# Performance work log

Measured on AMD Instinct MI355X. Metric: run time of the kernel, lower is better.

Reference implementation:

```python
import jax, jax.numpy as jnp
import numpy as np

B, Q, D = 8, 900, 256
NH, DH = 8, 32
FF = 1024
NLEVELS, NPOINTS, NLAYERS = 4, 4, 6
SHAPES = [(100, 100), (50, 50), (25, 25), (13, 13)]
S = sum(h * w for h, w in SHAPES)  # 13294
EPS = 1e-5
SCALE = 1.0 / float(np.sqrt(DH))


def layer_norm(x, g, b):
    mu = jnp.mean(x, -1, keepdims=True)
    var = jnp.var(x, -1, keepdims=True)
    return (x - mu) * jax.lax.rsqrt(var + EPS) * g + b


def mha(x, wi, bi, wo, bo):
    qkv = x @ wi.T + bi
    q, k, v = jnp.split(qkv, 3, axis=-1)
    q = q.reshape(B, Q, NH, DH)
    k = k.reshape(B, Q, NH, DH)
    v = v.reshape(B, Q, NH, DH)
    attn = jax.nn.softmax(jnp.einsum('bqhd,bkhd->bhqk', q, k) * SCALE, -1)
    o = jnp.einsum('bhqk,bkhd->bqhd', attn, v).reshape(B, Q, D)
    return o @ wo.T + bo


def msda_core(value, loc, aw):
    # value (B,S,NH,DH); loc (B,Q,NH,L,P,2) in [0,1]; aw (B,Q,NH,L,P)
    v = value.transpose(0, 2, 1, 3)  # (B,NH,S,DH)
    out = jnp.zeros((B, NH, Q, DH), value.dtype)
    start = 0
    for lvl, (H_, W_) in enumerate(SHAPES):
        vl = v[:, :, start:start + H_ * W_]  # (B,NH,HW,DH)
        start += H_ * W_
        l = loc[:, :, :, lvl].transpose(0, 2, 1, 3, 4).reshape(B, NH, Q * NPOINTS, 2)
        # grid_sample align_corners=False pixel coords
        x = l[..., 0] * W_ - 0.5
        y = l[..., 1] * H_ - 0.5
        x0 = jnp.floor(x)
        y0 = jnp.floor(y)
        wx = x - x0
        wy = y - y0
        g = jnp.zeros((B, NH, Q * NPOINTS, DH), value.dtype)
        for dy, dx, w in ((0, 0, (1 - wx) * (1 - wy)), (0, 1, wx * (1 - wy)),
                          (1, 0, (1 - wx) * wy), (1, 1, wx * wy)):
            xi = x0 + dx
            yi = y0 + dy
            valid = ((xi >= 0) & (xi < W_) & (yi >= 0) & (yi < H_)).astype(value.dtype)
            idx = (jnp.clip(yi, 0, H_ - 1) * W_ + jnp.clip(xi, 0, W_ - 1)).astype(jnp.int32)
            gi = jnp.take_along_axis(vl, idx[..., None], axis=2)  # (B,NH,QP,DH)
            g = g + gi * (w * valid)[..., None]
        g = g.reshape(B, NH, Q, NPOINTS, DH)
        a = aw[:, :, :, lvl].transpose(0, 2, 1, 3)  # (B,NH,Q,P)
        out = out + jnp.einsum('bhqpd,bhqp->bhqd', g, a)
    return out.transpose(0, 2, 1, 3).reshape(B, Q, D)


def msda(query, ref, value_in, vp_w, vp_b, so_w, so_b, aw_w, aw_b, op_w, op_b):
    value = (value_in @ vp_w.T + vp_b).reshape(B, S, NH, DH)
    off = (query @ so_w.T + so_b).reshape(B, Q, NH, NLEVELS, NPOINTS, 2)
    aw = (query @ aw_w.T + aw_b).reshape(B, Q, NH, NLEVELS * NPOINTS)
    aw = jax.nn.softmax(aw, -1).reshape(B, Q, NH, NLEVELS, NPOINTS)
    # offset normalizer is (W, H) per level
    norm = jnp.array([[w, h] for h, w in SHAPES], jnp.float32)
    loc = ref[:, :, None, :, None, :] + off / norm[None, None, None, :, None, :]
    return msda_core(value, loc, aw) @ op_w.T + op_b


def setup_inputs():
    key = jax.random.key(0)
    it = iter(jax.random.split(key, 32))

    def rn(shape, s=0.02):
        return jax.random.normal(next(it), shape, jnp.float32) * s

    z = lambda n: jnp.zeros((n,), jnp.float32)
    o = lambda n: jnp.ones((n,), jnp.float32)
    NOFF = NH * NLEVELS * NPOINTS
    return {
        'tgt': rn((B, Q, D), 1.0),
        'reference_points': jax.random.uniform(next(it), (B, Q, 2), jnp.float32),
        'memory': rn((B, S, D), 1.0),
        'spatial_shapes': jnp.array(SHAPES, jnp.int32),
        'level_start_index': jnp.array(np.cumsum([0] + [h * w for h, w in SHAPES[:-1]]), jnp.int32),
        'valid_ratios': jnp.ones((B, NLEVELS, 2), jnp.float32),
        'query_pos': rn((B, Q, D), 1.0),
        'sa_in_w': rn((3 * D, D)), 'sa_in_b': z(3 * D),
        'sa_out_w': rn((D, D)), 'sa_out_b': z(D),
        'n1_g': o(D), 'n1_b': z(D),
        'n2_g': o(D), 'n2_b': z(D),
        'n3_g': o(D), 'n3_b': z(D),
        'vp_w': rn((D, D)), 'vp_b': z(D),
        'so_w': rn((NOFF * 2, D)), 'so_b': rn((NOFF * 2,), 0.5),
        'aw_w': rn((NOFF, D)), 'aw_b': z(NOFF),
        'op_w': rn((D, D)), 'op_b': z(D),
        'ff1_w': rn((FF, D)), 'ff1_b': z(FF),
        'ff2_w': rn((D, FF)), 'ff2_b': z(D),
    }


def reference(tgt, reference_points, memory, spatial_shapes, level_start_index,
              valid_ratios, query_pos,
              sa_in_w, sa_in_b, sa_out_w, sa_out_b,
              n1_g, n1_b, n2_g, n2_b, n3_g, n3_b,
              vp_w, vp_b, so_w, so_b, aw_w, aw_b, op_w, op_b,
              ff1_w, ff1_b, ff2_w, ff2_b):
    # NOTE: nn.ModuleList([decoder_layer]*num_layers) in the source shares one
    # layer's weights across all 6 layers; bbox_embed is None so reference
    # points are constant across layers.
    output = tgt
    ref_input = reference_points[:, :, None, :] * valid_ratios[:, None, :, :]  # (B,Q,L,2)
    inter, inter_refs = [], []
    for _ in range(NLAYERS):
        output = output + query_pos
        t2 = mha(output, sa_in_w, sa_in_b, sa_out_w, sa_out_b)
        output = layer_norm(output + t2, n1_g, n1_b)
        t2 = msda(output, ref_input, memory, vp_w, vp_b, so_w, so_b, aw_w, aw_b, op_w, op_b)
        output = layer_norm(output + t2, n2_g, n2_b)
        t2 = jax.nn.relu(output @ ff1_w.T + ff1_b) @ ff2_w.T + ff2_b
        output = layer_norm(output + t2, n3_g, n3_b)
        inter.append(output)
        inter_refs.append(reference_points)
    return (jnp.stack(inter), jnp.stack(inter_refs))
```

## Files before the change

kernel.cpp:

```cpp
#include <hip/hip_runtime.h>
#include <hip/hip_bf16.h>

typedef __hip_bfloat16 bf16;
typedef __bf16 bf16x8 __attribute__((ext_vector_type(8)));
typedef float  f32x4  __attribute__((ext_vector_type(4)));

#define NB 8
#define NQ 900
#define DM 256
#define NHEADS 8
#define DHEAD 32
#define NFF 1024
#define NLAY 6
#define NS 13294
#define BQ (NB*NQ)
#define LN_EPS 1e-5f
#define ATT_SCALE 0.17677669529663687f
#define SAK 40
#define VWS 264
#define PSK 88

__device__ __forceinline__ float bfd(const bf16* p, size_t i){ return __bfloat162float(p[i]); }

__device__ __forceinline__ float ldv(const void* p, size_t i, int mode, bool extF32)
{
    if (mode == 0) return ((const float*)p)[i];
    if (mode == 1) return bfd((const bf16*)p, i);
    return extF32 ? ((const float*)p)[i] : bfd((const bf16*)p, i);
}

__device__ __forceinline__ void unpack8(uint4 u, float* t)
{
    t[0] = __uint_as_float((u.x & 0xffffu) << 16);
    t[1] = __uint_as_float(u.x & 0xffff0000u);
    t[2] = __uint_as_float((u.y & 0xffffu) << 16);
    t[3] = __uint_as_float(u.y & 0xffff0000u);
    t[4] = __uint_as_float((u.z & 0xffffu) << 16);
    t[5] = __uint_as_float(u.z & 0xffff0000u);
    t[6] = __uint_as_float((u.w & 0xffffu) << 16);
    t[7] = __uint_as_float(u.w & 0xffff0000u);
}

__global__ __launch_bounds__(256) void detect_dtype(const void* __restrict__ tgt,
        float* __restrict__ flag)
{
    __shared__ float red[256];
    int t = threadIdx.x;
    const unsigned short* u = (const unsigned short*)tgt;
    float m = 0.f;
    for (int i = t; i < 2048; i += 256) {
        unsigned int bits = ((unsigned int)u[i]) << 16;
        float v = fabsf(__uint_as_float(bits));
        if (!isfinite(v)) v = 1e30f;
        m = fmaxf(m, v);
    }
    red[t] = m;
    __syncthreads();
    for (int st = 128; st; st >>= 1) {
        if (t < st) red[t] = fmaxf(red[t], red[t + st]);
        __syncthreads();
    }
    if (t == 0) flag[0] = (red[0] > 1e8f) ? 1.f : 0.f;
}

__global__ __launch_bounds__(256) void convert_w(const void* __restrict__ src,
        bf16* __restrict__ dst, const float* __restrict__ flagp)
{
    const bool ef = flagp[0] > 0.5f;
    size_t base = ((size_t)blockIdx.x * 256 + threadIdx.x) * 8;
    if (ef) {
        const float* s = (const float*)src + base;
        float4 f0 = *(const float4*)s;
        float4 f1 = *(const float4*)(s + 4);
        union { bf16 a[8]; uint4 u; } t;
        t.a[0] = __float2bfloat16(f0.x); t.a[1] = __float2bfloat16(f0.y);
        t.a[2] = __float2bfloat16(f0.z); t.a[3] = __float2bfloat16(f0.w);
        t.a[4] = __float2bfloat16(f1.x); t.a[5] = __float2bfloat16(f1.y);
        t.a[6] = __float2bfloat16(f1.z); t.a[7] = __float2bfloat16(f1.w);
        *(uint4*)(dst + base) = t.u;
    } else {
        *(uint4*)(dst + base) = *(const uint4*)((const bf16*)src + base);
    }
}

__global__ __launch_bounds__(256, 2) void gemm_vp(const void* __restrict__ A,
        const bf16* __restrict__ Wb, const void* __restrict__ bias,
        bf16* __restrict__ C, int M, const float* __restrict__ flagp)
{
    const bool ef = flagp[0] > 0.5f;
    __shared__ __align__(16) bf16 Al[64 * VWS];
    const int tid = threadIdx.x;
    const int w = tid >> 6, lane = tid & 63, lm = lane & 15, lq = lane >> 4;
    const int wq = w * 64;

    bf16x8 wf[4][8];
    #pragma unroll
    for (int nt = 0; nt < 4; nt++)
        #pragma unroll
        for (int ks = 0; ks < 8; ks++)
            wf[nt][ks] = *(const bf16x8*)(Wb +
                (size_t)(wq + nt * 16 + lm) * 256 + ks * 32 + lq * 8);

    float bv[4];
    #pragma unroll
    for (int nt = 0; nt < 4; nt++) bv[nt] = ldv(bias, wq + nt * 16 + lm, 2, ef);

    const int arow_l = tid >> 2;
    const int asub   = tid & 3;

    const int ntiles = (M + 63) / 64;
    for (int tile = blockIdx.x; tile < ntiles; tile += gridDim.x) {
        const int m0 = tile * 64;
        __syncthreads();
        {
            const int grow = m0 + arow_l;
            if (grow < M) {
                if (ef) {
                    const float* ap = (const float*)A + (size_t)grow * 256;
                    #pragma unroll
                    for (int j = 0; j < 16; j++) {
                        int colf = j * 16 + asub * 4;
                        float4 f = *(const float4*)(ap + colf);
                        union { bf16 a[4]; uint2 u; } t;
                        t.a[0] = __float2bfloat16(f.x); t.a[1] = __float2bfloat16(f.y);
                        t.a[2] = __float2bfloat16(f.z); t.a[3] = __float2bfloat16(f.w);
                        *(uint2*)&Al[arow_l * VWS + colf] = t.u;
                    }
                } else {
                    const bf16* ap = (const bf16*)A + (size_t)grow * 256;
                    #pragma unroll
                    for (int j = 0; j < 8; j++) {
                        int cole = j * 32 + asub * 8;
                        *(uint4*)&Al[arow_l * VWS + cole] = *(const uint4*)(ap + cole);
                    }
                }
            } else {
                uint4 z = make_uint4(0u, 0u, 0u, 0u);
                #pragma unroll
                for (int j = 0; j < 8; j++)
                    *(uint4*)&Al[arow_l * VWS + j * 32 + asub * 8] = z;
            }
        }
        __syncthreads();

        f32x4 acc[4][4];
        #pragma unroll
        for (int mi = 0; mi < 4; mi++)
            #pragma unroll
            for (int nt = 0; nt < 4; nt++)
                acc[mi][nt] = (f32x4){0.f, 0.f, 0.f, 0.f};

        #pragma unroll
        for (int ks = 0; ks < 8; ks++) {
            bf16x8 af[4];
            #pragma unroll
            for (int mi = 0; mi < 4; mi++)
                af[mi] = *(const bf16x8*)&Al[(mi * 16 + lm) * VWS + ks * 32 + lq * 8];
            #pragma unroll
            for (int nt = 0; nt < 4; nt++)
                #pragma unroll
                for (int mi = 0; mi < 4; mi++)
                    acc[mi][nt] = __builtin_amdgcn_mfma_f32_16x16x32_bf16(
                                      af[mi], wf[nt][ks], acc[mi][nt], 0, 0, 0);
        }

        #pragma unroll
        for (int mi = 0; mi < 4; mi++) {
            #pragma unroll
            for (int r = 0; r < 4; r++) {
                int m = m0 + mi * 16 + lq * 4 + r;
                if (m >= M) continue;
                #pragma unroll
                for (int nt = 0; nt < 4; nt++) {
                    int col = wq + nt * 16 + lm;
                    C[(size_t)m * 256 + col] = __float2bfloat16(acc[mi][nt][r] + bv[nt]);
                }
            }
        }
    }
}

__device__ __forceinline__ void stage_a32(bf16* As, const void* A, bool a_bf16,
        int m0, int M, int K, int k0, int tid)
{
    const int row = tid >> 3, col = (tid & 7) * 4;
    const int arow = m0 + row;
    union { bf16 a[4]; uint2 u; } t;
    if (arow < M) {
        size_t base = (size_t)arow * K + k0 + col;
        if (a_bf16) {
            t.u = *(const uint2*)((const bf16*)A + base);
        } else {
            float4 f = *(const float4*)((const float*)A + base);
            t.a[0] = __float2bfloat16(f.x); t.a[1] = __float2bfloat16(f.y);
            t.a[2] = __float2bfloat16(f.z); t.a[3] = __float2bfloat16(f.w);
        }
    } else {
        t.u = make_uint2(0u, 0u);
    }
    *(uint2*)&As[row * SAK + col] = t.u;
}

__global__ __launch_bounds__(256) void gemm_a(const void* __restrict__ A, int amode,
        const bf16* __restrict__ Wb, const void* __restrict__ bias,
        void* __restrict__ C, int cmode, int M, int N, int K, int relu,
        const float* __restrict__ flagp)
{
    const bool ef = flagp[0] > 0.5f;
    const bool a_bf16 = (amode == 1) || (amode == 2 && !ef);
    __shared__ __align__(16) bf16 As[32 * SAK];
    __shared__ __align__(16) bf16 Ws[256 * SAK];
    const int tid = threadIdx.x;
    const int m0 = blockIdx.y * 32, n0 = blockIdx.x * 256;
    const int w = tid >> 6, lane = tid & 63, lm = lane & 15, lq = lane >> 4;
    const int wr = w >> 1, wc = w & 1;
    const int srow = tid >> 2, scol = (tid & 3) * 8;

    f32x4 acc[8];
    #pragma unroll
    for (int nt = 0; nt < 8; nt++) acc[nt] = (f32x4){0.f, 0.f, 0.f, 0.f};

    for (int k0 = 0; k0 < K; k0 += 32) {
        stage_a32(As, A, a_bf16, m0, M, K, k0, tid);
        #pragma unroll
        for (int it = 0; it < 4; it++) {
            int rr = it * 64 + srow;
            *(uint4*)&Ws[rr * SAK + scol] =
                *(const uint4*)(Wb + (size_t)(n0 + rr) * K + k0 + scol);
        }
        __syncthreads();

        bf16x8 af = *(const bf16x8*)&As[(wr * 16 + lm) * SAK + lq * 8];
        #pragma unroll
        for (int nt = 0; nt < 8; nt++) {
            bf16x8 bfr = *(const bf16x8*)&Ws[(wc * 128 + nt * 16 + lm) * SAK + lq * 8];
            acc[nt] = __builtin_amdgcn_mfma_f32_16x16x32_bf16(af, bfr, acc[nt], 0, 0, 0);
        }
        __syncthreads();
    }

    #pragma unroll
    for (int nt = 0; nt < 8; nt++) {
        int n = n0 + wc * 128 + nt * 16 + lm;
        float bv = ldv(bias, n, 2, ef);
        #pragma unroll
        for (int r = 0; r < 4; r++) {
            int m = m0 + wr * 16 + lq * 4 + r;
            if (m >= M) continue;
            float v = acc[nt][r] + bv;
            if (relu) v = fmaxf(v, 0.f);
            size_t ci = (size_t)m * N + n;
            if (cmode == 0) ((float*)C)[ci] = v;
            else            ((bf16*)C)[ci] = __float2bfloat16(v);
        }
    }
}

__global__ __launch_bounds__(256) void gemm_ln(const bf16* __restrict__ A,
        const bf16* __restrict__ Wb, const void* __restrict__ bias,
        const float* __restrict__ res, const void* __restrict__ gw,
        const void* __restrict__ bw, float* __restrict__ out32,
        bf16* __restrict__ outbf, void* __restrict__ dout, size_t obase,
        const void* __restrict__ qp, int M, int K,
        const float* __restrict__ flagp)
{
    const bool ef = flagp[0] > 0.5f;
    __shared__ __align__(16) bf16 As[32 * SAK];
    __shared__ __align__(16) bf16 Ws[256 * SAK];
    const int tid = threadIdx.x;
    const int m0 = blockIdx.y * 32;
    const int w = tid >> 6, lane = tid & 63, lm = lane & 15, lq = lane >> 4;
    const int wr = w >> 1, wc = w & 1;
    const int srow = tid >> 2, scol = (tid & 3) * 8;

    f32x4 acc[8];
    #pragma unroll
    for (int nt = 0; nt < 8; nt++) acc[nt] = (f32x4){0.f, 0.f, 0.f, 0.f};

    for (int k0 = 0; k0 < K; k0 += 32) {
        stage_a32(As, A, true, m0, M, K, k0, tid);
        #pragma unroll
        for (int it = 0; it < 4; it++) {
            int rr = it * 64 + srow;
            *(uint4*)&Ws[rr * SAK + scol] =
                *(const uint4*)(Wb + (size_t)rr * K + k0 + scol);
        }
        __syncthreads();

        bf16x8 af = *(const bf16x8*)&As[(wr * 16 + lm) * SAK + lq * 8];
        #pragma unroll
        for (int nt = 0; nt < 8; nt++) {
            bf16x8 bfr = *(const bf16x8*)&Ws[(wc * 128 + nt * 16 + lm) * SAK + lq * 8];
            acc[nt] = __builtin_amdgcn_mfma_f32_16x16x32_bf16(af, bfr, acc[nt], 0, 0, 0);
        }
        __syncthreads();
    }

    float bias_c[8], gcol[8], bcol[8];
    #pragma unroll
    for (int nt = 0; nt < 8; nt++) {
        int col = wc * 128 + nt * 16 + lm;
        bias_c[nt] = ldv(bias, col, 2, ef);
        gcol[nt]   = ldv(gw,   col, 2, ef);
        bcol[nt]   = ldv(bw,   col, 2, ef);
    }
    #pragma unroll
    for (int r = 0; r < 4; r++) {
        int row = m0 + wr * 16 + lq * 4 + r;
        bool vr_ = row < M;
        #pragma unroll
        for (int nt = 0; nt < 8; nt++) {
            int col = wc * 128 + nt * 16 + lm;
            float rv = vr_ ? res[(size_t)row * DM + col] : 0.f;
            acc[nt][r] += bias_c[nt] + rv;
        }
    }

    float* red = (float*)As;
    float mu[4], rstd[4];
    #pragma unroll
    for (int r = 0; r < 4; r++) {
        float s = 0.f;
        #pragma unroll
        for (int nt = 0; nt < 8; nt++) s += acc[nt][r];
        s += __shfl_xor(s, 1, 64); s += __shfl_xor(s, 2, 64);
        s += __shfl_xor(s, 4, 64); s += __shfl_xor(s, 8, 64);
        if (lm == 0) red[(wr * 16 + lq * 4 + r) * 2 + wc] = s;
    }
    __syncthreads();
    #pragma unroll
    for (int r = 0; r < 4; r++) {
        int rl = wr * 16 + lq * 4 + r;
        mu[r] = (red[rl * 2] + red[rl * 2 + 1]) * (1.f / DM);
    }
    #pragma unroll
    for (int r = 0; r < 4; r++) {
        float q = 0.f;
        #pragma unroll
        for (int nt = 0; nt < 8; nt++) {
            float d = acc[nt][r] - mu[r];
            q += d * d;
        }
        q += __shfl_xor(q, 1, 64); q += __shfl_xor(q, 2, 64);
        q += __shfl_xor(q, 4, 64); q += __shfl_xor(q, 8, 64);
        if (lm == 0) red[64 + (wr * 16 + lq * 4 + r) * 2 + wc] = q;
    }
    __syncthreads();
    #pragma unroll
    for (int r = 0; r < 4; r++) {
        int rl = wr * 16 + lq * 4 + r;
        float var = (red[64 + rl * 2] + red[64 + rl * 2 + 1]) * (1.f / DM);
        rstd[r] = rsqrtf(var + LN_EPS);
    }

    #pragma unroll
    for (int r = 0; r < 4; r++) {
        int row = m0 + wr * 16 + lq * 4 + r;
        if (row >= M) continue;
        size_t rbase = (size_t)row * DM;
        #pragma unroll
        for (int nt = 0; nt < 8; nt++) {
            int col = wc * 128 + nt * 16 + lm;
            float o = (acc[nt][r] - mu[r]) * rstd[r] * gcol[nt] + bcol[nt];
            if (dout) {
                if (ef) ((float*)dout)[obase + rbase + col] = o;
                else    ((bf16*)dout)[obase + rbase + col] = __float2bfloat16(o);
            }
            float o2 = o + (qp ? ldv(qp, rbase + col, 2, ef) : 0.f);
            out32[rbase + col] = o2;
            outbf[rbase + col] = __float2bfloat16(o2);
        }
    }
}

__global__ __launch_bounds__(256) void gemm_soaw(const bf16* __restrict__ A,
        const bf16* __restrict__ Wb, const void* __restrict__ b1,
        const void* __restrict__ b2, float* __restrict__ C1,
        float* __restrict__ C2, int M, const float* __restrict__ flagp)
{
    const bool ef = flagp[0] > 0.5f;
    const int K = DM;
    __shared__ __align__(16) bf16 As[32 * SAK];
    __shared__ __align__(16) bf16 Ws[128 * SAK];
    const int tid = threadIdx.x;
    const int m0 = blockIdx.y * 32, n0 = blockIdx.x * 128;
    const int w = tid >> 6, lane = tid & 63, lm = lane & 15, lq = lane >> 4;
    const int wr = w >> 1, wc = w & 1;
    const int srow = tid >> 2, scol = (tid & 3) * 8;

    f32x4 acc[4];
    #pragma unroll
    for (int nt = 0; nt < 4; nt++) acc[nt] = (f32x4){0.f, 0.f, 0.f, 0.f};

    for (int k0 = 0; k0 < K; k0 += 32) {
        stage_a32(As, A, true, m0, M, K, k0, tid);
        #pragma unroll
        for (int it = 0; it < 2; it++) {
            int rr = it * 64 + srow;
            *(uint4*)&Ws[rr * SAK + scol] =
                *(const uint4*)(Wb + (size_t)(n0 + rr) * K + k0 + scol);
        }
        __syncthreads();

        bf16x8 af = *(const bf16x8*)&As[(wr * 16 + lm) * SAK + lq * 8];
        #pragma unroll
        for (int nt = 0; nt < 4; nt++) {
            bf16x8 bfr = *(const bf16x8*)&Ws[(wc * 64 + nt * 16 + lm) * SAK + lq * 8];
            acc[nt] = __builtin_amdgcn_mfma_f32_16x16x32_bf16(af, bfr, acc[nt], 0, 0, 0);
        }
        __syncthreads();
    }

    float* Cd; const void* bsrc; int nst, c0;
    if (n0 < 256) { Cd = C1; bsrc = b1; nst = 256; c0 = n0; }
    else          { Cd = C2; bsrc = b2; nst = 128; c0 = n0 - 256; }

    #pragma unroll
    for (int nt = 0; nt < 4; nt++) {
        int cl = wc * 64 + nt * 16 + lm;
        float bv = ldv(bsrc, c0 + cl, 2, ef);
        #pragma unroll
        for (int r = 0; r < 4; r++) {
            int m = m0 + wr * 16 + lq * 4 + r;
            if (m >= M) continue;
            Cd[(size_t)m * nst + c0 + cl] = acc[nt][r] + bv;
        }
    }
}

__global__ __launch_bounds__(256) void add_qpos(const void* __restrict__ a, int amode,
        const void* __restrict__ qp, float* __restrict__ o, bf16* __restrict__ ob,
        const float* __restrict__ flagp)
{
    const bool ef = flagp[0] > 0.5f;
    int i = blockIdx.x * 256 + threadIdx.x;
    float v = ldv(a, i, amode, ef) + ldv(qp, i, 2, ef);
    o[i]  = v;
    ob[i] = __float2bfloat16(v);
}

__global__ __launch_bounds__(256) void mha_mfma(const bf16* __restrict__ qkv,
        bf16* __restrict__ out)
{
    const int qt = blockIdx.x, h = blockIdx.y, b = blockIdx.z;
    const int q0 = qt * 64;
    const int tid = threadIdx.x;
    const int w = tid >> 6, lane = tid & 63;
    const int lm = lane & 15, lq = lane >> 4;
    const int srow = tid >> 2, sc = (tid & 3) * 8;

    __shared__ __align__(16) bf16 Qs[64][SAK];
    __shared__ __align__(16) bf16 Ks[64][SAK];
    __shared__ __align__(16) bf16 Vt[32][66];
    __shared__ __align__(16) bf16 Ps[64][PSK];

    const bf16* base = qkv + (size_t)b * NQ * 768;

    {
        bf16 tmp[8];
        if (q0 + srow < NQ) {
            uint4 u = *(const uint4*)(base + (size_t)(q0 + srow) * 768 + h * DHEAD + sc);
            float t[8]; unpack8(u, t);
            #pragma unroll
            for (int i = 0; i < 8; i++) tmp[i] = __float2bfloat16(t[i] * ATT_SCALE);
        } else {
            #pragma unroll
            for (int i = 0; i < 8; i++) tmp[i] = __float2bfloat16(0.f);
        }
        *(uint4*)&Qs[srow][sc] = *(const uint4*)tmp;
    }
    __syncthreads();
    const bf16x8 qf = *(const bf16x8*)&Qs[w * 16 + lm][lq * 8];

    f32x4 O[2] = {{0.f,0.f,0.f,0.f},{0.f,0.f,0.f,0.f}};
    float mrow = -1e30f, lrow = 0.f;

    for (int k0 = 0; k0 < NQ; k0 += 64) {
        __syncthreads();
        {
            uint4 uk = {0u,0u,0u,0u}, uv = {0u,0u,0u,0u};
            if (k0 + srow < NQ) {
                const bf16* rp = base + (size_t)(k0 + srow) * 768 + h * DHEAD + sc;
                uk = *(const uint4*)(rp + 256);
                uv = *(const uint4*)(rp + 512);
            }
            *(uint4*)&Ks[srow][sc] = uk;
            const bf16* vv = (const bf16*)&uv;
            #pragma unroll
            for (int i = 0; i < 8; i++) Vt[sc + i][srow] = vv[i];
        }
        __syncthreads();

        float sv[16];
        #pragma unroll
        for (int mt = 0; mt < 4; mt++) {
            bf16x8 kf = *(const bf16x8*)&Ks[mt * 16 + lm][lq * 8];
            f32x4 d = __builtin_amdgcn_mfma_f32_16x16x32_bf16(kf, qf,
                        (f32x4){0.f,0.f,0.f,0.f}, 0, 0, 0);
            sv[mt*4+0] = d[0]; sv[mt*4+1] = d[1]; sv[mt*4+2] = d[2]; sv[mt*4+3] = d[3];
        }
        #pragma unroll
        for (int mt = 0; mt < 4; mt++)
            #pragma unroll
            for (int r = 0; r < 4; r++)
                if (k0 + mt * 16 + lq * 4 + r >= NQ) sv[mt*4+r] = -1e30f;

        float tmax = sv[0];
        #pragma unroll
        for (int j = 1; j < 16; j++) tmax = fmaxf(tmax, sv[j]);
        tmax = fmaxf(tmax, __shfl_xor(tmax, 16, 64));
        tmax = fmaxf(tmax, __shfl_xor(tmax, 32, 64));
        float mnew = fmaxf(mrow, tmax);
        float alpha = __expf(mrow - mnew);
        mrow = mnew;
        float psum = 0.f;
        #pragma unroll
        for (int j = 0; j < 16; j++) {
            float p = __expf(sv[j] - mnew);
            sv[j] = p; psum += p;
        }
        psum += __shfl_xor(psum, 16, 64);
        psum += __shfl_xor(psum, 32, 64);
        lrow = lrow * alpha + psum;

        #pragma unroll
        for (int mt = 0; mt < 4; mt++) {
            union { bf16 a[4]; uint2 u; } pw;
            #pragma unroll
            for (int r = 0; r < 4; r++) pw.a[r] = __float2bfloat16(sv[mt*4+r]);
            *(uint2*)&Ps[w * 16 + lm][mt * 16 + lq * 4] = pw.u;
        }

        #pragma unroll
        for (int mt = 0; mt < 2; mt++)
            #pragma unroll
            for (int r = 0; r < 4; r++) O[mt][r] *= alpha;
        #pragma unroll
        for (int ks = 0; ks < 2; ks++) {
            bf16x8 pf = *(const bf16x8*)&Ps[w * 16 + lm][ks * 32 + lq * 8];
            #pragma unroll
            for (int mt = 0; mt < 2; mt++) {
                bf16x8 vf = *(const bf16x8*)&Vt[mt * 16 + lm][ks * 32 + lq * 8];
                O[mt] = __builtin_amdgcn_mfma_f32_16x16x32_bf16(vf, pf, O[mt], 0, 0, 0);
            }
        }
    }

    int q = q0 + w * 16 + lm;
    if (q < NQ) {
        float invl = 1.f / lrow;
        bf16* op = out + ((size_t)(b * NQ + q)) * DM + h * DHEAD;
        #pragma unroll
        for (int mt = 0; mt < 2; mt++)
            #pragma unroll
            for (int r = 0; r < 4; r++)
                op[mt * 16 + lq * 4 + r] = __float2bfloat16(O[mt][r] * invl);
    }
}

__global__ __launch_bounds__(256) void msda_sample8(const bf16* __restrict__ value,
        const float* __restrict__ off, const float* __restrict__ aw,
        const void* __restrict__ refp, const void* __restrict__ vr,
        bf16* __restrict__ out, const float* __restrict__ flagp)
{
    const bool ef = flagp[0] > 0.5f;
    const int tid = threadIdx.x;
    const int bq0 = blockIdx.x * 8;

    __shared__ float sOff[8][256];
    __shared__ float sAw[8][128];
    __shared__ float sref[8][2];
    __shared__ float svrq[8][8];

    {
        const float* osrc = off + (size_t)bq0 * 256;
        #pragma unroll
        for (int i = 0; i < 2; i++) {
            int e = i * 1024 + tid * 4;
            *(float4*)&sOff[e >> 8][e & 255] = *(const float4*)(osrc + e);
        }
        int e2 = tid * 4;
        *(float4*)&sAw[e2 >> 7][e2 & 127] = *(const float4*)(aw + (size_t)bq0 * 128 + e2);
    }
    if (tid < 16) sref[tid >> 1][tid & 1] = ldv(refp, (size_t)(bq0 + (tid >> 1)) * 2 + (tid & 1), 2, ef);
    if (tid < 64) {
        int qi = tid >> 3, j = tid & 7;
        int b = (bq0 + qi) / NQ;
        svrq[qi][j] = ldv(vr, b * 8 + j, 2, ef);
    }
    __syncthreads();

    if (tid < 64) {
        int qi = tid >> 3, h = tid & 7;
        float* p = &sAw[qi][h * 16];
        float mx = -1e30f;
        #pragma unroll
        for (int j = 0; j < 16; j++) mx = fmaxf(mx, p[j]);
        float s = 0.f;
        #pragma unroll
        for (int j = 0; j < 16; j++) { float e = __expf(p[j] - mx); p[j] = e; s += e; }
        float inv = 1.f / s;
        #pragma unroll
        for (int j = 0; j < 16; j++) p[j] *= inv;
    }
    __syncthreads();

    const int qi = tid >> 5, sub = tid & 31;
    const int h = sub >> 2, cg = sub & 3;
    const int bq = bq0 + qi;
    const int b = bq / NQ;
    const bf16* vb = value + (size_t)b * NS * DM + h * DHEAD + cg * 8;

    float acc[8];
    #pragma unroll
    for (int j = 0; j < 8; j++) acc[j] = 0.f;

    const int HS[4] = {100, 50, 25, 13};
    const int ST[4] = {0, 10000, 12500, 13125};
    #pragma unroll
    for (int lvl = 0; lvl < 4; lvl++) {
        const int W_ = HS[lvl], H_ = HS[lvl], st = ST[lvl];
        float rx = sref[qi][0] * svrq[qi][lvl * 2 + 0] * (float)W_;
        float ry = sref[qi][1] * svrq[qi][lvl * 2 + 1] * (float)H_;
        #pragma unroll
        for (int p = 0; p < 4; p++) {
            int oi = h * 32 + lvl * 8 + p * 2;
            float x = fminf(fmaxf(rx + sOff[qi][oi]     - 0.5f, -4.f), (float)W_ + 4.f);
            float y = fminf(fmaxf(ry + sOff[qi][oi + 1] - 0.5f, -4.f), (float)H_ + 4.f);
            float x0f = floorf(x), y0f = floorf(y);
            float wx = x - x0f, wy = y - y0f;
            int x0 = (int)x0f, y0 = (int)y0f;
            int x1i = x0 + 1, y1i = y0 + 1;
            bool vx0 = (x0 >= 0) && (x0 < W_), vx1 = (x1i >= 0) && (x1i < W_);
            bool vy0 = (y0 >= 0) && (y0 < H_), vy1 = (y1i >= 0) && (y1i < H_);
            float g[8];
            #pragma unroll
            for (int j = 0; j < 8; j++) g[j] = 0.f;
            float t[8];
            if (vy0) {
                int rowo = (st + y0 * W_) * DM;
                if (vx0) {
                    uint4 u = *(const uint4*)(vb + rowo + x0 * DM);
                    unpack8(u, t);
                    float wgt = (1.f - wx) * (1.f - wy);
                    #pragma unroll
                    for (int j = 0; j < 8; j++) g[j] += wgt * t[j];
                }
                if (vx1) {
                    uint4 u = *(const uint4*)(vb + rowo + x1i * DM);
                    unpack8(u, t);
                    float wgt = wx * (1.f - wy);
                    #pragma unroll
                    for (int j = 0; j < 8; j++) g[j] += wgt * t[j];
                }
            }
            if (vy1) {
                int rowo = (st + y1i * W_) * DM;
                if (vx0) {
                    uint4 u = *(const uint4*)(vb + rowo + x0 * DM);
                    unpack8(u, t);
                    float wgt = (1.f - wx) * wy;
                    #pragma unroll
                    for (int j = 0; j < 8; j++) g[j] += wgt * t[j];
                }
                if (vx1) {
                    uint4 u = *(const uint4*)(vb + rowo + x1i * DM);
                    unpack8(u, t);
                    float wgt = wx * wy;
                    #pragma unroll
                    for (int j = 0; j < 8; j++) g[j] += wgt * t[j];
                }
            }
            float a = sAw[qi][h * 16 + lvl * 4 + p];
            #pragma unroll
            for (int j = 0; j < 8; j++) acc[j] += a * g[j];
        }
    }

    union { bf16 t[8]; uint4 u; } pk;
    #pragma unroll
    for (int j = 0; j < 8; j++) pk.t[j] = __float2bfloat16(acc[j]);
    *(uint4*)(out + (size_t)bq * DM + h * DHEAD + cg * 8) = pk.u;
}

__global__ __launch_bounds__(256) void copy_refs(const void* __restrict__ refp,
        void* __restrict__ out, const float* __restrict__ flagp)
{
    const bool ef = flagp[0] > 0.5f;
    int i = blockIdx.x * 256 + threadIdx.x;
    if (i >= NLAY * BQ * 2) return;
    float v = ldv(refp, i % (BQ * 2), 2, ef);
    size_t oi = (size_t)NLAY * BQ * DM + i;
    if (ef) ((float*)out)[oi] = v;
    else    ((bf16*)out)[oi] = __float2bfloat16(v);
}

extern "C" void kernel_launch(void* const* d_in, const int* in_sizes, int n_in,
                              void* d_out, int out_size, void* d_ws, size_t ws_size,
                              hipStream_t stream)
{
    const void* tgt     = d_in[0];
    const void* refp    = d_in[1];
    const void* memory  = d_in[2];
    const void* vr      = d_in[5];
    const void* qp      = d_in[6];
    const void* sa_in_w = d_in[7];
    const void* sa_in_b = d_in[8];
    const void* sa_out_w= d_in[9];
    const void* sa_out_b= d_in[10];
    const void* n1_g    = d_in[11];
    const void* n1_b    = d_in[12];
    const void* n2_g    = d_in[13];
    const void* n2_b    = d_in[14];
    const void* n3_g    = d_in[15];
    const void* n3_b    = d_in[16];
    const void* vp_w    = d_in[17];
    const void* vp_b    = d_in[18];
    const void* so_w    = d_in[19];
    const void* so_b    = d_in[20];
    const void* aw_w    = d_in[21];
    const void* aw_b    = d_in[22];
    const void* op_w    = d_in[23];
    const void* op_b    = d_in[24];
    const void* ff1_w   = d_in[25];
    const void* ff1_b   = d_in[26];
    const void* ff2_w   = d_in[27];
    const void* ff2_b   = d_in[28];

    char* w = (char*)d_ws;
    float* flagp  = (float*)w;  w += 256;
    bf16*  value  = (bf16*)w;   w += (size_t)NB * NS * DM * 2;
    float* outbuf = (float*)w;  w += (size_t)BQ * DM * 4;
    float* x1samp = (float*)w;  w += (size_t)BQ * DM * 4;
    bf16*  bigb   = (bf16*)w;   w += (size_t)BQ * NFF * 2;
    float* attoff = (float*)w;  w += (size_t)BQ * DM * 4;
    float* awb    = (float*)w;  w += (size_t)BQ * 128 * 4;
    bf16*  abuf   = (bf16*)w;   w += (size_t)BQ * DM * 2;
    bf16*  outbf  = (bf16*)w;   w += (size_t)BQ * DM * 2;
    bf16* wb_sa_in = (bf16*)w;  w += (size_t)768 * 256 * 2;
    bf16* wb_sa_out= (bf16*)w;  w += (size_t)256 * 256 * 2;
    bf16* wb_soaw  = (bf16*)w;  w += (size_t)384 * 256 * 2;
    bf16* wb_op    = (bf16*)w;  w += (size_t)256 * 256 * 2;
    bf16* wb_ff1   = (bf16*)w;  w += (size_t)NFF * 256 * 2;
    bf16* wb_ff2   = (bf16*)w;  w += (size_t)256 * NFF * 2;
    bf16* wb_vp    = (bf16*)w;  w += (size_t)256 * 256 * 2;

    const int gy = (BQ + 31) / 32;
    const int MV = NB * NS;

    detect_dtype<<<1, 256, 0, stream>>>(tgt, flagp);
    convert_w<<< 96, 256, 0, stream>>>(sa_in_w,  wb_sa_in,  flagp);
    convert_w<<< 32, 256, 0, stream>>>(sa_out_w, wb_sa_out, flagp);
    convert_w<<< 32, 256, 0, stream>>>(so_w,     wb_soaw,   flagp);
    convert_w<<< 16, 256, 0, stream>>>(aw_w,     wb_soaw + 256 * 256, flagp);
    convert_w<<< 32, 256, 0, stream>>>(op_w,     wb_op,     flagp);
    convert_w<<<128, 256, 0, stream>>>(ff1_w,    wb_ff1,    flagp);
    convert_w<<<128, 256, 0, stream>>>(ff2_w,    wb_ff2,    flagp);
    convert_w<<< 32, 256, 0, stream>>>(vp_w,     wb_vp,     flagp);

    gemm_vp<<<512, 256, 0, stream>>>(memory, wb_vp, vp_b, value, MV, flagp);

    copy_refs<<<(NLAY * BQ * 2 + 255) / 256, 256, 0, stream>>>(refp, d_out, flagp);

    add_qpos<<<BQ * DM / 256, 256, 0, stream>>>(tgt, 2, qp, x1samp, abuf, flagp);

    for (int l = 0; l < NLAY; l++) {
        gemm_a<<<dim3(768/256, gy), 256, 0, stream>>>(
            abuf, 1, wb_sa_in, sa_in_b, bigb, 1, BQ, 768, DM, 0, flagp);
        mha_mfma<<<dim3(15, NHEADS, NB), 256, 0, stream>>>(bigb, abuf);
        gemm_ln<<<dim3(1, gy), 256, 0, stream>>>(
            abuf, wb_sa_out, sa_out_b, x1samp, n1_g, n1_b,
            outbuf, outbf, nullptr, 0, nullptr, BQ, DM, flagp);

        gemm_soaw<<<dim3(3, gy), 256, 0, stream>>>(
            outbf, wb_soaw, so_b, aw_b, attoff, awb, BQ, flagp);
        msda_sample8<<<BQ / 8, 256, 0, stream>>>(value, attoff, awb, refp, vr, abuf, flagp);
        gemm_ln<<<dim3(1, gy), 256, 0, stream>>>(
            abuf, wb_op, op_b, outbuf, n2_g, n2_b,
            outbuf, outbf, nullptr, 0, nullptr, BQ, DM, flagp);

        gemm_a<<<dim3(NFF/256, gy), 256, 0, stream>>>(
            outbf, 1, wb_ff1, ff1_b, bigb, 1, BQ, NFF, DM, 1, flagp);
        gemm_ln<<<dim3(1, gy), 256, 0, stream>>>(
            bigb, wb_ff2, ff2_b, outbuf, n3_g, n3_b,
            x1samp, abuf, d_out, (size_t)l * BQ * DM, qp, BQ, NFF, flagp);
    }
}
```

Baseline: 1.483 ms.

## Keep weight fragments in registers for K=256 GEMMs and fused LayerNorm GEMMs

Adds gemm_wreg and gemm_lnw kernels that load each wave's 64-column slice of the weight matrix (full K=256) into registers once. The 32-row A tile is staged into LDS in one pass, so the per-k-step LDS staging and barriers of the old gemm_a and gemm_ln loops go away. The QKV, FF1 and the two K=256 LN-fused projections use the new kernels, and gemm_a is removed. The trade-off is high register pressure (32 bf16x8 fragments per lane), and every M tile re-reads the weights from global or L2.

```diff
diff --git a/kernel.cpp b/kernel.cpp
--- a/kernel.cpp
+++ b/kernel.cpp
@@ -180,6 +180,238 @@
     }
 }
 
+__global__ __launch_bounds__(256, 2) void gemm_wreg(const bf16* __restrict__ A,
+        const bf16* __restrict__ Wb, const void* __restrict__ bias,
+        void* __restrict__ C, int cmode, int M, int N, int relu,
+        const float* __restrict__ flagp)
+{
+    const bool ef = flagp[0] > 0.5f;
+    __shared__ __align__(16) bf16 Al[32 * VWS];
+    const int tid = threadIdx.x;
+    const int w = tid >> 6, lane = tid & 63, lm = lane & 15, lq = lane >> 4;
+    const int n0 = blockIdx.x * 256;
+    const int m0 = blockIdx.y * 32;
+    const int wq = n0 + w * 64;
+
+    bf16x8 wf[4][8];
+    #pragma unroll
+    for (int nt = 0; nt < 4; nt++)
+        #pragma unroll
+        for (int ks = 0; ks < 8; ks++)
+            wf[nt][ks] = *(const bf16x8*)(Wb +
+                (size_t)(wq + nt * 16 + lm) * 256 + ks * 32 + lq * 8);
+
+    float bv[4];
+    #pragma unroll
+    for (int nt = 0; nt < 4; nt++) bv[nt] = ldv(bias, wq + nt * 16 + lm, 2, ef);
+
+    {
+        const int ar = tid >> 3, ac = (tid & 7) * 32;
+        if (m0 + ar < M) {
+            const bf16* ap = A + (size_t)(m0 + ar) * 256 + ac;
+            #pragma unroll
+            for (int j = 0; j < 4; j++)
+                *(uint4*)&Al[ar * VWS + ac + j * 8] = *(const uint4*)(ap + j * 8);
+        } else {
+            uint4 z = make_uint4(0u, 0u, 0u, 0u);
+            #pragma unroll
+            for (int j = 0; j < 4; j++)
+                *(uint4*)&Al[ar * VWS + ac + j * 8] = z;
+        }
+    }
+    __syncthreads();
+
+    f32x4 acc[2][4];
+    #pragma unroll
+    for (int mi = 0; mi < 2; mi++)
+        #pragma unroll
+        for (int nt = 0; nt < 4; nt++)
+            acc[mi][nt] = (f32x4){0.f, 0.f, 0.f, 0.f};
+
+    #pragma unroll
+    for (int ks = 0; ks < 8; ks++) {
+        bf16x8 af[2];
+        #pragma unroll
+        for (int mi = 0; mi < 2; mi++)
+            af[mi] = *(const bf16x8*)&Al[(mi * 16 + lm) * VWS + ks * 32 + lq * 8];
+        #pragma unroll
+        for (int nt = 0; nt < 4; nt++)
+            #pragma unroll
+            for (int mi = 0; mi < 2; mi++)
+                acc[mi][nt] = __builtin_amdgcn_mfma_f32_16x16x32_bf16(
+                                  af[mi], wf[nt][ks], acc[mi][nt], 0, 0, 0);
+    }
+
+    #pragma unroll
+    for (int mi = 0; mi < 2; mi++) {
+        #pragma unroll
+        for (int r = 0; r < 4; r++) {
+            int m = m0 + mi * 16 + lq * 4 + r;
+            if (m >= M) continue;
+            #pragma unroll
+            for (int nt = 0; nt < 4; nt++) {
+                int col = wq + nt * 16 + lm;
+                float v = acc[mi][nt][r] + bv[nt];
+                if (relu) v = fmaxf(v, 0.f);
+                size_t ci = (size_t)m * N + col;
+                if (cmode == 0) ((float*)C)[ci] = v;
+                else            ((bf16*)C)[ci] = __float2bfloat16(v);
+            }
+        }
+    }
+}
+
+__global__ __launch_bounds__(256, 2) void gemm_lnw(const bf16* __restrict__ A,
+        const bf16* __restrict__ Wb, const void* __restrict__ bias,
+        const float* __restrict__ res, const void* __restrict__ gw,
+        const void* __restrict__ bw, float* __restrict__ out32,
+        bf16* __restrict__ outbf, void* __restrict__ dout, size_t obase,
+        const void* __restrict__ qp, int M,
+        const float* __restrict__ flagp)
+{
+    const bool ef = flagp[0] > 0.5f;
+    __shared__ __align__(16) bf16 Al[32 * VWS];
+    const int tid = threadIdx.x;
+    const int w = tid >> 6, lane = tid & 63, lm = lane & 15, lq = lane >> 4;
+    const int m0 = blockIdx.y * 32;
+    const int wq = w * 64;
+
+    bf16x8 wf[4][8];
+    #pragma unroll
+    for (int nt = 0; nt < 4; nt++)
+        #pragma unroll
+        for (int ks = 0; ks < 8; ks++)
+            wf[nt][ks] = *(const bf16x8*)(Wb +
+                (size_t)(wq + nt * 16 + lm) * 256 + ks * 32 + lq * 8);
+
+    float bias_c[4];
+    #pragma unroll
+    for (int nt = 0; nt < 4; nt++) bias_c[nt] = ldv(bias, wq + nt * 16 + lm, 2, ef);
+
+    {
+        const int ar = tid >> 3, ac = (tid & 7) * 32;
+        if (m0 + ar < M) {
+            const bf16* ap = A + (size_t)(m0 + ar) * 256 + ac;
+            #pragma unroll
+            for (int j = 0; j < 4; j++)
+                *(uint4*)&Al[ar * VWS + ac + j * 8] = *(const uint4*)(ap + j * 8);
+        } else {
+            uint4 z = make_uint4(0u, 0u, 0u, 0u);
+            #pragma unroll
+            for (int j = 0; j < 4; j++)
+                *(uint4*)&Al[ar * VWS + ac + j * 8] = z;
+        }
+    }
+    __syncthreads();
+
+    f32x4 acc[2][4];
+    #pragma unroll
+    for (int mi = 0; mi < 2; mi++)
+        #pragma unroll
+        for (int nt = 0; nt < 4; nt++)
+            acc[mi][nt] = (f32x4){0.f, 0.f, 0.f, 0.f};
+
+    #pragma unroll
+    for (int ks = 0; ks < 8; ks++) {
+        bf16x8 af[2];
+        #pragma unroll
+        for (int mi = 0; mi < 2; mi++)
+            af[mi] = *(const bf16x8*)&Al[(mi * 16 + lm) * VWS + ks * 32 + lq * 8];
+        #pragma unroll
+        for (int nt = 0; nt < 4; nt++)
+            #pragma unroll
+            for (int mi = 0; mi < 2; mi++)
+                acc[mi][nt] = __builtin_amdgcn_mfma_f32_16x16x32_bf16(
+                                  af[mi], wf[nt][ks], acc[mi][nt], 0, 0, 0);
+    }
+
+    #pragma unroll
+    for (int mi = 0; mi < 2; mi++)
+        #pragma unroll
+        for (int r = 0; r < 4; r++) {
+            int row = m0 + mi * 16 + lq * 4 + r;
+            bool vr_ = row < M;
+            #pragma unroll
+            for (int nt = 0; nt < 4; nt++) {
+                int col = wq + nt * 16 + lm;
+                float rv = vr_ ? res[(size_t)row * DM + col] : 0.f;
+                acc[mi][nt][r] += bias_c[nt] + rv;
+            }
+        }
+
+    __syncthreads();
+    float* red = (float*)Al;
+    float mu[2][4], rstd[2][4];
+    #pragma unroll
+    for (int mi = 0; mi < 2; mi++)
+        #pragma unroll
+        for (int r = 0; r < 4; r++) {
+            float s = acc[mi][0][r] + acc[mi][1][r] + acc[mi][2][r] + acc[mi][3][r];
+            s += __shfl_xor(s, 1, 64); s += __shfl_xor(s, 2, 64);
+            s += __shfl_xor(s, 4, 64); s += __shfl_xor(s, 8, 64);
+            if (lm == 0) red[(mi * 16 + lq * 4 + r) * 4 + w] = s;
+        }
+    __syncthreads();
+    #pragma unroll
+    for (int mi = 0; mi < 2; mi++)
+        #pragma unroll
+        for (int r = 0; r < 4; r++) {
+            int ri = mi * 16 + lq * 4 + r;
+            mu[mi][r] = (red[ri*4] + red[ri*4+1] + red[ri*4+2] + red[ri*4+3]) * (1.f / DM);
+        }
+    #pragma unroll
+    for (int mi = 0; mi < 2; mi++)
+        #pragma unroll
+        for (int r = 0; r < 4; r++) {
+            float q = 0.f;
+            #pragma unroll
+            for (int nt = 0; nt < 4; nt++) {
+                float d = acc[mi][nt][r] - mu[mi][r];
+                q += d * d;
+            }
+            q += __shfl_xor(q, 1, 64); q += __shfl_xor(q, 2, 64);
+            q += __shfl_xor(q, 4, 64); q += __shfl_xor(q, 8, 64);
+            if (lm == 0) red[128 + (mi * 16 + lq * 4 + r) * 4 + w] = q;
+        }
+    __syncthreads();
+    #pragma unroll
+    for (int mi = 0; mi < 2; mi++)
+        #pragma unroll
+        for (int r = 0; r < 4; r++) {
+            int ri = mi * 16 + lq * 4 + r;
+            float var = (red[128+ri*4] + red[128+ri*4+1] + red[128+ri*4+2] + red[128+ri*4+3]) * (1.f / DM);
+            rstd[mi][r] = rsqrtf(var + LN_EPS);
+        }
+
+    float gcol[4], bcol[4];
+    #pragma unroll
+    for (int nt = 0; nt < 4; nt++) {
+        int col = wq + nt * 16 + lm;
+        gcol[nt] = ldv(gw, col, 2, ef);
+        bcol[nt] = ldv(bw, col, 2, ef);
+    }
+    #pragma unroll
+    for (int mi = 0; mi < 2; mi++)
+        #pragma unroll
+        for (int r = 0; r < 4; r++) {
+            int row = m0 + mi * 16 + lq * 4 + r;
+            if (row >= M) continue;
+            size_t rbase = (size_t)row * DM;
+            #pragma unroll
+            for (int nt = 0; nt < 4; nt++) {
+                int col = wq + nt * 16 + lm;
+                float o = (acc[mi][nt][r] - mu[mi][r]) * rstd[mi][r] * gcol[nt] + bcol[nt];
+                if (dout) {
+                    if (ef) ((float*)dout)[obase + rbase + col] = o;
+                    else    ((bf16*)dout)[obase + rbase + col] = __float2bfloat16(o);
+                }
+                float o2 = o + (qp ? ldv(qp, rbase + col, 2, ef) : 0.f);
+                out32[rbase + col] = o2;
+                outbf[rbase + col] = __float2bfloat16(o2);
+            }
+        }
+}
+
 __device__ __forceinline__ void stage_a32(bf16* As, const void* A, bool a_bf16,
         int m0, int M, int K, int k0, int tid)
 {
@@ -199,61 +431,6 @@
         t.u = make_uint2(0u, 0u);
     }
     *(uint2*)&As[row * SAK + col] = t.u;
-}
-
-__global__ __launch_bounds__(256) void gemm_a(const void* __restrict__ A, int amode,
-        const bf16* __restrict__ Wb, const void* __restrict__ bias,
-        void* __restrict__ C, int cmode, int M, int N, int K, int relu,
-        const float* __restrict__ flagp)
-{
-    const bool ef = flagp[0] > 0.5f;
-    const bool a_bf16 = (amode == 1) || (amode == 2 && !ef);
-    __shared__ __align__(16) bf16 As[32 * SAK];
-    __shared__ __align__(16) bf16 Ws[256 * SAK];
-    const int tid = threadIdx.x;
-    const int m0 = blockIdx.y * 32, n0 = blockIdx.x * 256;
-    const int w = tid >> 6, lane = tid & 63, lm = lane & 15, lq = lane >> 4;
-    const int wr = w >> 1, wc = w & 1;
-    const int srow = tid >> 2, scol = (tid & 3) * 8;
-
-    f32x4 acc[8];
-    #pragma unroll
-    for (int nt = 0; nt < 8; nt++) acc[nt] = (f32x4){0.f, 0.f, 0.f, 0.f};
-
-    for (int k0 = 0; k0 < K; k0 += 32) {
-        stage_a32(As, A, a_bf16, m0, M, K, k0, tid);
-        #pragma unroll
-        for (int it = 0; it < 4; it++) {
-            int rr = it * 64 + srow;
-            *(uint4*)&Ws[rr * SAK + scol] =
-                *(const uint4*)(Wb + (size_t)(n0 + rr) * K + k0 + scol);
-        }
-        __syncthreads();
-
-        bf16x8 af = *(const bf16x8*)&As[(wr * 16 + lm) * SAK + lq * 8];
-        #pragma unroll
-        for (int nt = 0; nt < 8; nt++) {
-            bf16x8 bfr = *(const bf16x8*)&Ws[(wc * 128 + nt * 16 + lm) * SAK + lq * 8];
-            acc[nt] = __builtin_amdgcn_mfma_f32_16x16x32_bf16(af, bfr, acc[nt], 0, 0, 0);
-        }
-        __syncthreads();
-    }
-
-    #pragma unroll
-    for (int nt = 0; nt < 8; nt++) {
-        int n = n0 + wc * 128 + nt * 16 + lm;
-        float bv = ldv(bias, n, 2, ef);
-        #pragma unroll
-        for (int r = 0; r < 4; r++) {
-            int m = m0 + wr * 16 + lq * 4 + r;
-            if (m >= M) continue;
-            float v = acc[nt][r] + bv;
-            if (relu) v = fmaxf(v, 0.f);
-            size_t ci = (size_t)m * N + n;
-            if (cmode == 0) ((float*)C)[ci] = v;
-            else            ((bf16*)C)[ci] = __float2bfloat16(v);
-        }
-    }
 }
 
 __global__ __launch_bounds__(256) void gemm_ln(const bf16* __restrict__ A,
@@ -765,22 +942,22 @@
     add_qpos<<<BQ * DM / 256, 256, 0, stream>>>(tgt, 2, qp, x1samp, abuf, flagp);
 
     for (int l = 0; l < NLAY; l++) {
-        gemm_a<<<dim3(768/256, gy), 256, 0, stream>>>(
-            abuf, 1, wb_sa_in, sa_in_b, bigb, 1, BQ, 768, DM, 0, flagp);
+        gemm_wreg<<<dim3(3, gy), 256, 0, stream>>>(
+            abuf, wb_sa_in, sa_in_b, bigb, 1, BQ, 768, 0, flagp);
         mha_mfma<<<dim3(15, NHEADS, NB), 256, 0, stream>>>(bigb, abuf);
-        gemm_ln<<<dim3(1, gy), 256, 0, stream>>>(
+        gemm_lnw<<<dim3(1, gy), 256, 0, stream>>>(
             abuf, wb_sa_out, sa_out_b, x1samp, n1_g, n1_b,
-            outbuf, outbf, nullptr, 0, nullptr, BQ, DM, flagp);
+            outbuf, outbf, nullptr, 0, nullptr, BQ, flagp);
 
         gemm_soaw<<<dim3(3, gy), 256, 0, stream>>>(
             outbf, wb_soaw, so_b, aw_b, attoff, awb, BQ, flagp);
         msda_sample8<<<BQ / 8, 256, 0, stream>>>(value, attoff, awb, refp, vr, abuf, flagp);
-        gemm_ln<<<dim3(1, gy), 256, 0, stream>>>(
+        gemm_lnw<<<dim3(1, gy), 256, 0, stream>>>(
             abuf, wb_op, op_b, outbuf, n2_g, n2_b,
-            outbuf, outbf, nullptr, 0, nullptr, BQ, DM, flagp);
-
-        gemm_a<<<dim3(NFF/256, gy), 256, 0, stream>>>(
-            outbf, 1, wb_ff1, ff1_b, bigb, 1, BQ, NFF, DM, 1, flagp);
+            outbuf, outbf, nullptr, 0, nullptr, BQ, flagp);
+
+        gemm_wreg<<<dim3(4, gy), 256, 0, stream>>>(
+            outbf, wb_ff1, ff1_b, bigb, 1, BQ, 1024, 1, flagp);
         gemm_ln<<<dim3(1, gy), 256, 0, stream>>>(
             bigb, wb_ff2, ff2_b, outbuf, n3_g, n3_b,
             x1samp, abuf, d_out, (size_t)l * BQ * DM, qp, BQ, NFF, flagp);
```

Measured after the change: 1.486 ms. Within noise of the previous version (+0.2%).
